# Optimization experiments

Hardware: AMD Instinct MI355X
Metric: run time of the kernel (lower is better)

The kernel has to match this reference:

```python
import jax, jax.numpy as jnp
import numpy as np

B, MENU, N, M = 4096, 256, 8, 16


def setup_inputs() -> dict:
    key = jax.random.key(0)
    k1, k2, k3, k4 = jax.random.split(key, 4)
    input_bids = jax.random.uniform(k1, (B, N, M), dtype=jnp.float32)
    allocs = jax.random.uniform(k2, (B, MENU, N, M), dtype=jnp.float32)
    # bidder weights must be strictly positive (divided by in payments)
    w = jax.random.uniform(k3, (B, N), dtype=jnp.float32, minval=0.5, maxval=1.5)
    b = jax.random.normal(k4, (B, MENU), dtype=jnp.float32)
    softmax_temp = jnp.asarray(100.0, dtype=jnp.float32)
    return {"input_bids": input_bids, "allocs": allocs, "w": w, "b": b,
            "softmax_temp": softmax_temp}


def reference(input_bids, allocs, w, b, softmax_temp):
    Bsz, n, m = input_bids.shape
    # append the "null" menu entry (zero allocation, zero boost)
    allocs = jnp.concatenate([allocs, jnp.zeros((Bsz, 1, n, m), allocs.dtype)], axis=1)  # B,S,n,m
    b = jnp.concatenate([b, jnp.zeros((Bsz, 1), b.dtype)], axis=1)                        # B,S

    # utility of each agent under each menu entry
    util = jnp.einsum('bsnm,bnm->bsn', allocs, input_bids)        # B,S,n
    per_agent_welfare = w[:, None, :] * util                      # B,S,n
    total_welfare = per_agent_welfare.sum(-1)                     # B,S

    alloc_choice = jax.nn.softmax((total_welfare + b) * softmax_temp, axis=-1)  # B,S
    item_allocation = jnp.einsum('bs,bsnm->bnm', alloc_choice, allocs)          # B,n,m
    chosen_welfare = jnp.einsum('bsn,bs->bn', per_agent_welfare, alloc_choice)  # B,n

    # leave-one-out (VCG-style) payments, vectorized over the removed agent i
    mask = 1.0 - jnp.eye(n, dtype=per_agent_welfare.dtype)        # n,n; row i zeros agent i
    removed_welfare = per_agent_welfare[None] * mask[:, None, None, :]  # i,B,S,n
    total_removed = removed_welfare.sum(-1)                       # i,B,S
    removed_choice = jax.nn.softmax((total_removed + b[None]) * softmax_temp, axis=-1)  # i,B,S

    removed_chosen_sum = jnp.einsum('ibsn,ibs->ib', removed_welfare, removed_choice)  # i,B
    masked_chosen_sum = jnp.einsum('bn,in->ib', chosen_welfare, mask)                 # i,B
    removed_b = jnp.einsum('ibs,bs->ib', removed_choice, b)                           # i,B
    alloc_b = jnp.einsum('bs,bs->b', alloc_choice, b)                                 # B

    payments = (removed_chosen_sum + removed_b - masked_chosen_sum - alloc_b[None]) / w.T  # n,B
    return alloc_choice, item_allocation, payments, allocs
```

## Files before the change

### kernel.cpp

```cpp
#include <hip/hip_runtime.h>

#define NAGENTS 8
#define MITEMS 16
#define NM 128
#define MENU 256
#define SFULL 257

__device__ __forceinline__ float wredmax(float v) {
#pragma unroll
    for (int o = 32; o; o >>= 1) v = fmaxf(v, __shfl_xor(v, o));
    return v;
}
__device__ __forceinline__ float wredsum(float v) {
#pragma unroll
    for (int o = 32; o; o >>= 1) v += __shfl_xor(v, o);
    return v;
}

__global__ __launch_bounds__(1024) void cama_kernel(
    const float* __restrict__ bids,
    const float* __restrict__ allocs,
    const float* __restrict__ wvec,
    const float* __restrict__ bvec,
    const float* __restrict__ tempp,
    float* __restrict__ out, int Bsz)
{
    __shared__ float4 lda4[MENU * 32];
    __shared__ float lds_pwT[NAGENTS * MENU];
    __shared__ float lds_tot[MENU];
    __shared__ float lds_bb[MENU];
    __shared__ __align__(16) float lds_bids[NM];
    __shared__ float lds_w[NAGENTS];
    __shared__ float lds_ch[SFULL];
    __shared__ float lds_rcs[NAGENTS], lds_rb[NAGENTS], lds_cw[NAGENTS];
    __shared__ float lds_ab;

    const int u = threadIdx.x;
    const int lane = u & 63;
    const int wave = u >> 6;
    const int b = blockIdx.x;
    const size_t bb = (size_t)b;

    float* out_choice = out;
    float* out_item   = out + (size_t)Bsz * SFULL;
    float* out_pay    = out_item + (size_t)Bsz * NM;
    float* out_all    = out_pay + (size_t)NAGENTS * Bsz;

    if (u < NM) lds_bids[u] = bids[bb * NM + u];
    else if (u < NM + NAGENTS) lds_w[u - NM] = wvec[bb * NAGENTS + (u - NM)];
    if (u >= 256 && u < 512) lds_bb[u - 256] = bvec[bb * MENU + (u - 256)];
    __syncthreads();

    const float temp = tempp[0];
    const int n = u & 7;
    const float w_n = lds_w[n];
    const float4* bq = (const float4*)lds_bids + (n << 2);
    const float4 q0 = bq[0], q1 = bq[1], q2 = bq[2], q3 = bq[3];

#pragma unroll
    for (int i = 0; i < 2; ++i) {
        const int s = (i << 7) + (u >> 3);
        const float4* src = (const float4*)(allocs + ((bb << 8) + s) * NM) + (n << 2);
        float4 a0 = src[0], a1 = src[1], a2 = src[2], a3 = src[3];
        float4* dst = (float4*)(out_all + (bb * SFULL + s) * NM) + (n << 2);
        dst[0] = a0; dst[1] = a1; dst[2] = a2; dst[3] = a3;
        float util = a0.x*q0.x + a0.y*q0.y + a0.z*q0.z + a0.w*q0.w
                   + a1.x*q1.x + a1.y*q1.y + a1.z*q1.z + a1.w*q1.w
                   + a2.x*q2.x + a2.y*q2.y + a2.z*q2.z + a2.w*q2.w
                   + a3.x*q3.x + a3.y*q3.y + a3.z*q3.z + a3.w*q3.w;
        float pwv = w_n * util;
        lds_pwT[(n << 8) + s] = pwv;
        float t4 = pwv;
        t4 += __shfl_xor(t4, 1);
        t4 += __shfl_xor(t4, 2);
        t4 += __shfl_xor(t4, 4);
        if (n == 0) lds_tot[s] = t4;
        const int base = s << 5, c7 = s & 7, j0 = n << 2;
        lda4[base + ((j0 + 0) ^ c7)] = a0;
        lda4[base + ((j0 + 1) ^ c7)] = a1;
        lda4[base + ((j0 + 2) ^ c7)] = a2;
        lda4[base + ((j0 + 3) ^ c7)] = a3;
    }
    if (u < 32) {
        float4 z = make_float4(0.f, 0.f, 0.f, 0.f);
        ((float4*)(out_all + (bb * SFULL + MENU) * NM))[u] = z;
    }
    __syncthreads();

    if (wave == 0) {
        float xs[4], bl[4], es[4];
        float mx = -1e30f;
#pragma unroll
        for (int c = 0; c < 4; ++c) {
            int v = (c << 6) | lane;
            bl[c] = lds_bb[v];
            float x = (lds_tot[v] + bl[c]) * temp;
            xs[c] = x; mx = fmaxf(mx, x);
        }
        mx = fmaxf(wredmax(mx), 0.f);
        float se = 0.f, sab = 0.f;
#pragma unroll
        for (int c = 0; c < 4; ++c) { es[c] = __expf(xs[c] - mx); se += es[c]; sab += es[c] * bl[c]; }
        float en = __expf(-mx);
        se = wredsum(se) + en;
        sab = wredsum(sab);
        float inv = 1.f / se;
#pragma unroll
        for (int c = 0; c < 4; ++c) {
            int v = (c << 6) | lane;
            float chv = es[c] * inv;
            lds_ch[v] = chv;
            out_choice[bb * SFULL + v] = chv;
        }
        if (lane == 0) {
            float chn = en * inv;
            lds_ch[MENU] = chn;
            out_choice[bb * SFULL + MENU] = chn;
            lds_ab = sab * inv;
        }
    } else if (wave <= 8) {
        const int i = wave - 1;
        float xs[4], trs[4], bl[4];
        float mx = -1e30f;
#pragma unroll
        for (int c = 0; c < 4; ++c) {
            int v = (c << 6) | lane;
            bl[c] = lds_bb[v];
            float tr = lds_tot[v] - lds_pwT[(i << 8) + v];
            trs[c] = tr;
            float x = (tr + bl[c]) * temp;
            xs[c] = x; mx = fmaxf(mx, x);
        }
        mx = fmaxf(wredmax(mx), 0.f);
        float se = 0.f, s1 = 0.f, s2 = 0.f;
#pragma unroll
        for (int c = 0; c < 4; ++c) {
            float e = __expf(xs[c] - mx);
            se += e; s1 += e * trs[c]; s2 += e * bl[c];
        }
        se = wredsum(se) + __expf(-mx);
        s1 = wredsum(s1);
        s2 = wredsum(s2);
        if (lane == 0) { lds_rcs[i] = s1 / se; lds_rb[i] = s2 / se; }
    }
    __syncthreads();

    if (wave < 8) {
        float cwv = 0.f;
#pragma unroll
        for (int c = 0; c < 4; ++c) {
            int v = (c << 6) | lane;
            cwv += lds_ch[v] * lds_pwT[(wave << 8) + v];
        }
        cwv = wredsum(cwv);
        if (lane == 0) lds_cw[wave] = cwv;
    }
    {
        const float* ldf = (const float*)lda4;
        const int wl = lane & 7, chunk = lane >> 3;
        const int nm = (wave << 3) + wl;
        const int jj = nm >> 2, r = nm & 3;
        float acc = 0.f;
#pragma unroll 4
        for (int it = 0; it < 32; ++it) {
            int s = (it << 3) + chunk;
            float av = ldf[(((s << 5) + (jj ^ (s & 7))) << 2) + r];
            acc += lds_ch[s] * av;
        }
        acc += __shfl_xor(acc, 8);
        acc += __shfl_xor(acc, 16);
        acc += __shfl_xor(acc, 32);
        if (chunk == 0) out_item[bb * NM + nm] = acc;
    }
    __syncthreads();

    if (u < NAGENTS) {
        float ctot = 0.f;
#pragma unroll
        for (int k = 0; k < NAGENTS; ++k) ctot += lds_cw[k];
        float pay = (lds_rcs[u] + lds_rb[u] - (ctot - lds_cw[u]) - lds_ab) / lds_w[u];
        out_pay[(size_t)u * Bsz + b] = pay;
    }
}

extern "C" void kernel_launch(void* const* d_in, const int* in_sizes, int n_in,
                              void* d_out, int out_size, void* d_ws, size_t ws_size,
                              hipStream_t stream) {
    const float* bids   = (const float*)d_in[0];
    const float* allocs = (const float*)d_in[1];
    const float* wvec   = (const float*)d_in[2];
    const float* bvec   = (const float*)d_in[3];
    const float* tempp  = (const float*)d_in[4];
    float* out = (float*)d_out;
    const int Bsz = in_sizes[0] / (NAGENTS * MITEMS);
    cama_kernel<<<Bsz, 1024, 0, stream>>>(bids, allocs, wvec, bvec, tempp, out, Bsz);
}
```

Before: 268.7 us.

## Halve block size, keep half the menu in registers to shrink LDS

Each block now runs 512 threads instead of 1024. Every thread processes four menu rows instead of two. The first half of the allocation rows stays in registers and is reduced with shuffles into a scratch area, so the shared-memory tile holds only 128 rows and more blocks can fit per CU. The per-agent transposed welfare array gets an XOR swizzle to avoid bank conflicts. All eight waves now run the leave-one-out softmax, the main softmax runs on wave 0 in addition, and the item allocation is finished with an extra cross-wave reduction and barrier. The costs are more register pressure and an extra synchronisation step.

```diff
diff --git a/kernel.cpp b/kernel.cpp
--- a/kernel.cpp
+++ b/kernel.cpp
@@ -17,7 +17,7 @@
     return v;
 }
 
-__global__ __launch_bounds__(1024) void cama_kernel(
+__global__ __launch_bounds__(512, 4) void cama_kernel(
     const float* __restrict__ bids,
     const float* __restrict__ allocs,
     const float* __restrict__ wvec,
@@ -25,7 +25,7 @@
     const float* __restrict__ tempp,
     float* __restrict__ out, int Bsz)
 {
-    __shared__ float4 lda4[MENU * 32];
+    __shared__ float4 lda4[128 * 32];
     __shared__ float lds_pwT[NAGENTS * MENU];
     __shared__ float lds_tot[MENU];
     __shared__ float lds_bb[MENU];
@@ -38,6 +38,8 @@
     const int u = threadIdx.x;
     const int lane = u & 63;
     const int wave = u >> 6;
+    const int n = u & 7;
+    const int sg = u >> 3;
     const int b = blockIdx.x;
     const size_t bb = (size_t)b;
 
@@ -47,19 +49,20 @@
     float* out_all    = out_pay + (size_t)NAGENTS * Bsz;
 
     if (u < NM) lds_bids[u] = bids[bb * NM + u];
-    else if (u < NM + NAGENTS) lds_w[u - NM] = wvec[bb * NAGENTS + (u - NM)];
-    if (u >= 256 && u < 512) lds_bb[u - 256] = bvec[bb * MENU + (u - 256)];
+    if (u >= NM && u < NM + NAGENTS) lds_w[u - NM] = wvec[bb * NAGENTS + (u - NM)];
+    if (u >= 256) lds_bb[u - 256] = bvec[bb * MENU + (u - 256)];
     __syncthreads();
 
     const float temp = tempp[0];
-    const int n = u & 7;
     const float w_n = lds_w[n];
     const float4* bq = (const float4*)lds_bids + (n << 2);
     const float4 q0 = bq[0], q1 = bq[1], q2 = bq[2], q3 = bq[3];
 
-#pragma unroll
-    for (int i = 0; i < 2; ++i) {
-        const int s = (i << 7) + (u >> 3);
+    float4 P00, P01, P02, P03, P10, P11, P12, P13;
+
+#pragma unroll
+    for (int c = 0; c < 4; ++c) {
+        const int s = (c << 6) + sg;
         const float4* src = (const float4*)(allocs + ((bb << 8) + s) * NM) + (n << 2);
         float4 a0 = src[0], a1 = src[1], a2 = src[2], a3 = src[3];
         float4* dst = (float4*)(out_all + (bb * SFULL + s) * NM) + (n << 2);
@@ -69,17 +72,21 @@
                    + a2.x*q2.x + a2.y*q2.y + a2.z*q2.z + a2.w*q2.w
                    + a3.x*q3.x + a3.y*q3.y + a3.z*q3.z + a3.w*q3.w;
         float pwv = w_n * util;
-        lds_pwT[(n << 8) + s] = pwv;
+        lds_pwT[(n << 8) + (s ^ (n << 2))] = pwv;
         float t4 = pwv;
         t4 += __shfl_xor(t4, 1);
         t4 += __shfl_xor(t4, 2);
         t4 += __shfl_xor(t4, 4);
         if (n == 0) lds_tot[s] = t4;
-        const int base = s << 5, c7 = s & 7, j0 = n << 2;
-        lda4[base + ((j0 + 0) ^ c7)] = a0;
-        lda4[base + ((j0 + 1) ^ c7)] = a1;
-        lda4[base + ((j0 + 2) ^ c7)] = a2;
-        lda4[base + ((j0 + 3) ^ c7)] = a3;
+        if (c == 0)      { P00 = a0; P01 = a1; P02 = a2; P03 = a3; }
+        else if (c == 1) { P10 = a0; P11 = a1; P12 = a2; P13 = a3; }
+        else {
+            const int base = (s - 128) << 5, c7 = s & 7, j0 = n << 2;
+            lda4[base + ((j0 + 0) ^ c7)] = a0;
+            lda4[base + ((j0 + 1) ^ c7)] = a1;
+            lda4[base + ((j0 + 2) ^ c7)] = a2;
+            lda4[base + ((j0 + 3) ^ c7)] = a3;
+        }
     }
     if (u < 32) {
         float4 z = make_float4(0.f, 0.f, 0.f, 0.f);
@@ -118,15 +125,16 @@
             out_choice[bb * SFULL + MENU] = chn;
             lds_ab = sab * inv;
         }
-    } else if (wave <= 8) {
-        const int i = wave - 1;
+    }
+    {
+        const int i = wave;
         float xs[4], trs[4], bl[4];
         float mx = -1e30f;
 #pragma unroll
         for (int c = 0; c < 4; ++c) {
             int v = (c << 6) | lane;
             bl[c] = lds_bb[v];
-            float tr = lds_tot[v] - lds_pwT[(i << 8) + v];
+            float tr = lds_tot[v] - lds_pwT[(i << 8) + (v ^ (i << 2))];
             trs[c] = tr;
             float x = (tr + bl[c]) * temp;
             xs[c] = x; mx = fmaxf(mx, x);
@@ -145,35 +153,70 @@
     }
     __syncthreads();
 
-    if (wave < 8) {
+    {
+        const int i = wave;
         float cwv = 0.f;
 #pragma unroll
         for (int c = 0; c < 4; ++c) {
             int v = (c << 6) | lane;
-            cwv += lds_ch[v] * lds_pwT[(wave << 8) + v];
+            cwv += lds_ch[v] * lds_pwT[(i << 8) + (v ^ (i << 2))];
         }
         cwv = wredsum(cwv);
-        if (lane == 0) lds_cw[wave] = cwv;
-    }
-    {
+        if (lane == 0) lds_cw[i] = cwv;
+    }
+    __syncthreads();
+
+    float* scratchA = lds_pwT;
+    float* scratchB = lds_pwT + 1024;
+    {
+        float c0 = lds_ch[sg], c1 = lds_ch[64 + sg];
+        float vs[16];
+        vs[ 0] = P00.x*c0 + P10.x*c1;  vs[ 1] = P00.y*c0 + P10.y*c1;
+        vs[ 2] = P00.z*c0 + P10.z*c1;  vs[ 3] = P00.w*c0 + P10.w*c1;
+        vs[ 4] = P01.x*c0 + P11.x*c1;  vs[ 5] = P01.y*c0 + P11.y*c1;
+        vs[ 6] = P01.z*c0 + P11.z*c1;  vs[ 7] = P01.w*c0 + P11.w*c1;
+        vs[ 8] = P02.x*c0 + P12.x*c1;  vs[ 9] = P02.y*c0 + P12.y*c1;
+        vs[10] = P02.z*c0 + P12.z*c1;  vs[11] = P02.w*c0 + P12.w*c1;
+        vs[12] = P03.x*c0 + P13.x*c1;  vs[13] = P03.y*c0 + P13.y*c1;
+        vs[14] = P03.z*c0 + P13.z*c1;  vs[15] = P03.w*c0 + P13.w*c1;
+#pragma unroll
+        for (int wd = 0; wd < 16; ++wd) {
+            float t = vs[wd];
+            t += __shfl_xor(t, 8);
+            t += __shfl_xor(t, 16);
+            t += __shfl_xor(t, 32);
+            vs[wd] = t;
+        }
+        if (lane < 8) {
+            float4* d4 = (float4*)(scratchA + (wave << 7) + (lane << 4));
+            d4[0] = make_float4(vs[ 0], vs[ 1], vs[ 2], vs[ 3]);
+            d4[1] = make_float4(vs[ 4], vs[ 5], vs[ 6], vs[ 7]);
+            d4[2] = make_float4(vs[ 8], vs[ 9], vs[10], vs[11]);
+            d4[3] = make_float4(vs[12], vs[13], vs[14], vs[15]);
+        }
+    }
+    {
+        const int nm = u & 127, k = u >> 7;
+        const int jj = nm >> 2, r = nm & 3;
         const float* ldf = (const float*)lda4;
-        const int wl = lane & 7, chunk = lane >> 3;
-        const int nm = (wave << 3) + wl;
-        const int jj = nm >> 2, r = nm & 3;
         float acc = 0.f;
-#pragma unroll 4
+#pragma unroll 8
         for (int it = 0; it < 32; ++it) {
-            int s = (it << 3) + chunk;
-            float av = ldf[(((s << 5) + (jj ^ (s & 7))) << 2) + r];
-            acc += lds_ch[s] * av;
-        }
-        acc += __shfl_xor(acc, 8);
-        acc += __shfl_xor(acc, 16);
-        acc += __shfl_xor(acc, 32);
-        if (chunk == 0) out_item[bb * NM + nm] = acc;
-    }
-    __syncthreads();
-
+            int sl = (k << 5) + it;
+            acc += lds_ch[128 + sl] * ldf[(sl << 7) + (((jj ^ (sl & 7)) << 2) | r)];
+        }
+        scratchB[(k << 7) + nm] = acc;
+    }
+    __syncthreads();
+
+    if (u < NM) {
+        float sum = 0.f;
+#pragma unroll
+        for (int w = 0; w < 8; ++w) sum += scratchA[(w << 7) + u];
+#pragma unroll
+        for (int k = 0; k < 4; ++k) sum += scratchB[(k << 7) + u];
+        out_item[bb * NM + u] = sum;
+    }
     if (u < NAGENTS) {
         float ctot = 0.f;
 #pragma unroll
@@ -193,5 +236,5 @@
     const float* tempp  = (const float*)d_in[4];
     float* out = (float*)d_out;
     const int Bsz = in_sizes[0] / (NAGENTS * MITEMS);
-    cama_kernel<<<Bsz, 1024, 0, stream>>>(bids, allocs, wvec, bvec, tempp, out, Bsz);
-}
+    cama_kernel<<<Bsz, 512, 0, stream>>>(bids, allocs, wvec, bvec, tempp, out, Bsz);
+}
```

New measurement: 255.4 us. 4.9% less time.

## Make kernel persistent with register-prefetched next batch and double-buffered LDS

Applied to the files above, without the earlier changes.

Launches a fixed grid of 256 blocks that each loop over consecutive batch elements. While the current element is being processed, the next element's allocs, bids, w and b are loaded into registers, then staged into double-buffered LDS. The goal is to hide global load latency and cut block launch overhead. It also swizzles the lds_pwT index to reduce bank conflicts and replaces __syncthreads with a raw lgkmcnt wait plus s_barrier. In exchange, parallelism drops to 256 blocks on a large GPU, and iters = Bsz/256 silently drops any remainder when B is not a multiple of 256.

```diff
diff --git a/kernel.cpp b/kernel.cpp
--- a/kernel.cpp
+++ b/kernel.cpp
@@ -1,11 +1,12 @@
 #include <hip/hip_runtime.h>
 
 #define NAGENTS 8
-#define MITEMS 16
 #define NM 128
 #define MENU 256
 #define SFULL 257
 
+#define BAR() asm volatile("s_waitcnt lgkmcnt(0)\n\ts_barrier" ::: "memory")
+
 __device__ __forceinline__ float wredmax(float v) {
 #pragma unroll
     for (int o = 32; o; o >>= 1) v = fmaxf(v, __shfl_xor(v, o));
@@ -17,20 +18,20 @@
     return v;
 }
 
-__global__ __launch_bounds__(1024) void cama_kernel(
+__global__ __launch_bounds__(1024, 4) void cama_kernel(
     const float* __restrict__ bids,
     const float* __restrict__ allocs,
     const float* __restrict__ wvec,
     const float* __restrict__ bvec,
     const float* __restrict__ tempp,
-    float* __restrict__ out, int Bsz)
+    float* __restrict__ out, int Bsz, int iters)
 {
     __shared__ float4 lda4[MENU * 32];
     __shared__ float lds_pwT[NAGENTS * MENU];
     __shared__ float lds_tot[MENU];
-    __shared__ float lds_bb[MENU];
-    __shared__ __align__(16) float lds_bids[NM];
-    __shared__ float lds_w[NAGENTS];
+    __shared__ float lds_bb[2][MENU];
+    __shared__ __align__(16) float lds_bids[2][NM];
+    __shared__ float lds_w[2][NAGENTS];
     __shared__ float lds_ch[SFULL];
     __shared__ float lds_rcs[NAGENTS], lds_rb[NAGENTS], lds_cw[NAGENTS];
     __shared__ float lds_ab;
@@ -38,148 +39,208 @@
     const int u = threadIdx.x;
     const int lane = u & 63;
     const int wave = u >> 6;
-    const int b = blockIdx.x;
-    const size_t bb = (size_t)b;
+    const int n = u & 7;
+    const int sg = u >> 3;
 
     float* out_choice = out;
     float* out_item   = out + (size_t)Bsz * SFULL;
     float* out_pay    = out_item + (size_t)Bsz * NM;
     float* out_all    = out_pay + (size_t)NAGENTS * Bsz;
 
-    if (u < NM) lds_bids[u] = bids[bb * NM + u];
-    else if (u < NM + NAGENTS) lds_w[u - NM] = wvec[bb * NAGENTS + (u - NM)];
-    if (u >= 256 && u < 512) lds_bb[u - 256] = bvec[bb * MENU + (u - 256)];
-    __syncthreads();
-
     const float temp = tempp[0];
-    const int n = u & 7;
-    const float w_n = lds_w[n];
-    const float4* bq = (const float4*)lds_bids + (n << 2);
-    const float4 q0 = bq[0], q1 = bq[1], q2 = bq[2], q3 = bq[3];
-
-#pragma unroll
-    for (int i = 0; i < 2; ++i) {
-        const int s = (i << 7) + (u >> 3);
-        const float4* src = (const float4*)(allocs + ((bb << 8) + s) * NM) + (n << 2);
-        float4 a0 = src[0], a1 = src[1], a2 = src[2], a3 = src[3];
-        float4* dst = (float4*)(out_all + (bb * SFULL + s) * NM) + (n << 2);
-        dst[0] = a0; dst[1] = a1; dst[2] = a2; dst[3] = a3;
-        float util = a0.x*q0.x + a0.y*q0.y + a0.z*q0.z + a0.w*q0.w
-                   + a1.x*q1.x + a1.y*q1.y + a1.z*q1.z + a1.w*q1.w
-                   + a2.x*q2.x + a2.y*q2.y + a2.z*q2.z + a2.w*q2.w
-                   + a3.x*q3.x + a3.y*q3.y + a3.z*q3.z + a3.w*q3.w;
-        float pwv = w_n * util;
-        lds_pwT[(n << 8) + s] = pwv;
-        float t4 = pwv;
-        t4 += __shfl_xor(t4, 1);
-        t4 += __shfl_xor(t4, 2);
-        t4 += __shfl_xor(t4, 4);
-        if (n == 0) lds_tot[s] = t4;
-        const int base = s << 5, c7 = s & 7, j0 = n << 2;
-        lda4[base + ((j0 + 0) ^ c7)] = a0;
-        lda4[base + ((j0 + 1) ^ c7)] = a1;
-        lda4[base + ((j0 + 2) ^ c7)] = a2;
-        lda4[base + ((j0 + 3) ^ c7)] = a3;
+
+    size_t a = (size_t)blockIdx.x * iters;
+
+    float Pf[2][16];
+
+    {
+        float rbb = 0.f, rbid = 0.f, rw = 0.f;
+        if (u < MENU)    rbb  = bvec[a * MENU + u];
+        if (u < NM)      rbid = bids[a * NM + u];
+        if (u < NAGENTS) rw   = wvec[a * NAGENTS + u];
+        const float4* s0 = (const float4*)(allocs + (a * MENU + sg) * NM) + (n << 2);
+        const float4* s1 = (const float4*)(allocs + (a * MENU + 128 + sg) * NM) + (n << 2);
+        float4 a0 = s0[0], a1 = s0[1], a2 = s0[2], a3 = s0[3];
+        float4 b0 = s1[0], b1 = s1[1], b2 = s1[2], b3 = s1[3];
+        Pf[0][0]=a0.x;  Pf[0][1]=a0.y;  Pf[0][2]=a0.z;  Pf[0][3]=a0.w;
+        Pf[0][4]=a1.x;  Pf[0][5]=a1.y;  Pf[0][6]=a1.z;  Pf[0][7]=a1.w;
+        Pf[0][8]=a2.x;  Pf[0][9]=a2.y;  Pf[0][10]=a2.z; Pf[0][11]=a2.w;
+        Pf[0][12]=a3.x; Pf[0][13]=a3.y; Pf[0][14]=a3.z; Pf[0][15]=a3.w;
+        Pf[1][0]=b0.x;  Pf[1][1]=b0.y;  Pf[1][2]=b0.z;  Pf[1][3]=b0.w;
+        Pf[1][4]=b1.x;  Pf[1][5]=b1.y;  Pf[1][6]=b1.z;  Pf[1][7]=b1.w;
+        Pf[1][8]=b2.x;  Pf[1][9]=b2.y;  Pf[1][10]=b2.z; Pf[1][11]=b2.w;
+        Pf[1][12]=b3.x; Pf[1][13]=b3.y; Pf[1][14]=b3.z; Pf[1][15]=b3.w;
+        if (u < MENU)    lds_bb[0][u]   = rbb;
+        if (u < NM)      lds_bids[0][u] = rbid;
+        if (u < NAGENTS) lds_w[0][u]    = rw;
     }
-    if (u < 32) {
-        float4 z = make_float4(0.f, 0.f, 0.f, 0.f);
-        ((float4*)(out_all + (bb * SFULL + MENU) * NM))[u] = z;
-    }
-    __syncthreads();
-
-    if (wave == 0) {
-        float xs[4], bl[4], es[4];
-        float mx = -1e30f;
-#pragma unroll
-        for (int c = 0; c < 4; ++c) {
-            int v = (c << 6) | lane;
-            bl[c] = lds_bb[v];
-            float x = (lds_tot[v] + bl[c]) * temp;
-            xs[c] = x; mx = fmaxf(mx, x);
-        }
-        mx = fmaxf(wredmax(mx), 0.f);
-        float se = 0.f, sab = 0.f;
-#pragma unroll
-        for (int c = 0; c < 4; ++c) { es[c] = __expf(xs[c] - mx); se += es[c]; sab += es[c] * bl[c]; }
-        float en = __expf(-mx);
-        se = wredsum(se) + en;
-        sab = wredsum(sab);
-        float inv = 1.f / se;
-#pragma unroll
-        for (int c = 0; c < 4; ++c) {
-            int v = (c << 6) | lane;
-            float chv = es[c] * inv;
-            lds_ch[v] = chv;
-            out_choice[bb * SFULL + v] = chv;
-        }
-        if (lane == 0) {
-            float chn = en * inv;
-            lds_ch[MENU] = chn;
-            out_choice[bb * SFULL + MENU] = chn;
-            lds_ab = sab * inv;
-        }
-    } else if (wave <= 8) {
-        const int i = wave - 1;
-        float xs[4], trs[4], bl[4];
-        float mx = -1e30f;
-#pragma unroll
-        for (int c = 0; c < 4; ++c) {
-            int v = (c << 6) | lane;
-            bl[c] = lds_bb[v];
-            float tr = lds_tot[v] - lds_pwT[(i << 8) + v];
-            trs[c] = tr;
-            float x = (tr + bl[c]) * temp;
-            xs[c] = x; mx = fmaxf(mx, x);
-        }
-        mx = fmaxf(wredmax(mx), 0.f);
-        float se = 0.f, s1 = 0.f, s2 = 0.f;
-#pragma unroll
-        for (int c = 0; c < 4; ++c) {
-            float e = __expf(xs[c] - mx);
-            se += e; s1 += e * trs[c]; s2 += e * bl[c];
-        }
-        se = wredsum(se) + __expf(-mx);
-        s1 = wredsum(s1);
-        s2 = wredsum(s2);
-        if (lane == 0) { lds_rcs[i] = s1 / se; lds_rb[i] = s2 / se; }
-    }
-    __syncthreads();
-
-    if (wave < 8) {
-        float cwv = 0.f;
-#pragma unroll
-        for (int c = 0; c < 4; ++c) {
-            int v = (c << 6) | lane;
-            cwv += lds_ch[v] * lds_pwT[(wave << 8) + v];
-        }
-        cwv = wredsum(cwv);
-        if (lane == 0) lds_cw[wave] = cwv;
-    }
-    {
-        const float* ldf = (const float*)lda4;
-        const int wl = lane & 7, chunk = lane >> 3;
-        const int nm = (wave << 3) + wl;
-        const int jj = nm >> 2, r = nm & 3;
-        float acc = 0.f;
-#pragma unroll 4
-        for (int it = 0; it < 32; ++it) {
-            int s = (it << 3) + chunk;
-            float av = ldf[(((s << 5) + (jj ^ (s & 7))) << 2) + r];
-            acc += lds_ch[s] * av;
-        }
-        acc += __shfl_xor(acc, 8);
-        acc += __shfl_xor(acc, 16);
-        acc += __shfl_xor(acc, 32);
-        if (chunk == 0) out_item[bb * NM + nm] = acc;
-    }
-    __syncthreads();
-
-    if (u < NAGENTS) {
-        float ctot = 0.f;
-#pragma unroll
-        for (int k = 0; k < NAGENTS; ++k) ctot += lds_cw[k];
-        float pay = (lds_rcs[u] + lds_rb[u] - (ctot - lds_cw[u]) - lds_ab) / lds_w[u];
-        out_pay[(size_t)u * Bsz + b] = pay;
+    BAR();
+
+    for (int it = 0; it < iters; ++it) {
+        const int p = it & 1;
+
+        float qf[16];
+        {
+            const float4* bq = (const float4*)(&lds_bids[p][0]) + (n << 2);
+            float4 qa = bq[0], qb = bq[1], qc = bq[2], qd = bq[3];
+            qf[0]=qa.x; qf[1]=qa.y; qf[2]=qa.z; qf[3]=qa.w;
+            qf[4]=qb.x; qf[5]=qb.y; qf[6]=qb.z; qf[7]=qb.w;
+            qf[8]=qc.x; qf[9]=qc.y; qf[10]=qc.z; qf[11]=qc.w;
+            qf[12]=qd.x; qf[13]=qd.y; qf[14]=qd.z; qf[15]=qd.w;
+        }
+        const float w_n = lds_w[p][n];
+#pragma unroll
+        for (int c = 0; c < 2; ++c) {
+            const int s = (c << 7) + sg;
+            float4 v0 = make_float4(Pf[c][0],  Pf[c][1],  Pf[c][2],  Pf[c][3]);
+            float4 v1 = make_float4(Pf[c][4],  Pf[c][5],  Pf[c][6],  Pf[c][7]);
+            float4 v2 = make_float4(Pf[c][8],  Pf[c][9],  Pf[c][10], Pf[c][11]);
+            float4 v3 = make_float4(Pf[c][12], Pf[c][13], Pf[c][14], Pf[c][15]);
+            float4* dst = (float4*)(out_all + (a * SFULL + s) * NM) + (n << 2);
+            dst[0] = v0; dst[1] = v1; dst[2] = v2; dst[3] = v3;
+            float util = 0.f;
+#pragma unroll
+            for (int k = 0; k < 16; ++k) util += Pf[c][k] * qf[k];
+            float pwv = w_n * util;
+            lds_pwT[(n << 8) + (s ^ (n << 2))] = pwv;
+            float t4 = pwv;
+            t4 += __shfl_xor(t4, 1);
+            t4 += __shfl_xor(t4, 2);
+            t4 += __shfl_xor(t4, 4);
+            if (n == 0) lds_tot[s] = t4;
+            const int base = s << 5, c7 = s & 7, j0 = n << 2;
+            lda4[base + ((j0 + 0) ^ c7)] = v0;
+            lda4[base + ((j0 + 1) ^ c7)] = v1;
+            lda4[base + ((j0 + 2) ^ c7)] = v2;
+            lda4[base + ((j0 + 3) ^ c7)] = v3;
+        }
+        if (u < 32)
+            ((float4*)(out_all + (a * SFULL + MENU) * NM))[u] =
+                make_float4(0.f, 0.f, 0.f, 0.f);
+
+        const bool has_next = (it + 1 < iters);
+        const size_t an = a + 1;
+        float rbb2 = 0.f, rbid2 = 0.f, rw2 = 0.f;
+        if (has_next) {
+            if (u < MENU)    rbb2  = bvec[an * MENU + u];
+            if (u < NM)      rbid2 = bids[an * NM + u];
+            if (u < NAGENTS) rw2   = wvec[an * NAGENTS + u];
+            const float4* s0 = (const float4*)(allocs + (an * MENU + sg) * NM) + (n << 2);
+            const float4* s1 = (const float4*)(allocs + (an * MENU + 128 + sg) * NM) + (n << 2);
+            float4 a0 = s0[0], a1 = s0[1], a2 = s0[2], a3 = s0[3];
+            float4 b0 = s1[0], b1 = s1[1], b2 = s1[2], b3 = s1[3];
+            Pf[0][0]=a0.x;  Pf[0][1]=a0.y;  Pf[0][2]=a0.z;  Pf[0][3]=a0.w;
+            Pf[0][4]=a1.x;  Pf[0][5]=a1.y;  Pf[0][6]=a1.z;  Pf[0][7]=a1.w;
+            Pf[0][8]=a2.x;  Pf[0][9]=a2.y;  Pf[0][10]=a2.z; Pf[0][11]=a2.w;
+            Pf[0][12]=a3.x; Pf[0][13]=a3.y; Pf[0][14]=a3.z; Pf[0][15]=a3.w;
+            Pf[1][0]=b0.x;  Pf[1][1]=b0.y;  Pf[1][2]=b0.z;  Pf[1][3]=b0.w;
+            Pf[1][4]=b1.x;  Pf[1][5]=b1.y;  Pf[1][6]=b1.z;  Pf[1][7]=b1.w;
+            Pf[1][8]=b2.x;  Pf[1][9]=b2.y;  Pf[1][10]=b2.z; Pf[1][11]=b2.w;
+            Pf[1][12]=b3.x; Pf[1][13]=b3.y; Pf[1][14]=b3.z; Pf[1][15]=b3.w;
+        }
+        BAR();
+
+        if (wave == 0) {
+            float xs[4], bl[4], es[4];
+            float mx = -1e30f;
+#pragma unroll
+            for (int c = 0; c < 4; ++c) {
+                int v = (c << 6) | lane;
+                bl[c] = lds_bb[p][v];
+                float x = (lds_tot[v] + bl[c]) * temp;
+                xs[c] = x; mx = fmaxf(mx, x);
+            }
+            mx = fmaxf(wredmax(mx), 0.f);
+            float se = 0.f, sab = 0.f;
+#pragma unroll
+            for (int c = 0; c < 4; ++c) { es[c] = __expf(xs[c] - mx); se += es[c]; sab += es[c] * bl[c]; }
+            float en = __expf(-mx);
+            se = wredsum(se) + en;
+            sab = wredsum(sab);
+            float inv = 1.f / se;
+#pragma unroll
+            for (int c = 0; c < 4; ++c) {
+                int v = (c << 6) | lane;
+                float chv = es[c] * inv;
+                lds_ch[v] = chv;
+                out_choice[a * SFULL + v] = chv;
+            }
+            if (lane == 0) {
+                float chn = en * inv;
+                lds_ch[MENU] = chn;
+                out_choice[a * SFULL + MENU] = chn;
+                lds_ab = sab * inv;
+            }
+        } else if (wave <= 8) {
+            const int i = wave - 1;
+            float xs[4], trs[4], bl[4];
+            float mx = -1e30f;
+#pragma unroll
+            for (int c = 0; c < 4; ++c) {
+                int v = (c << 6) | lane;
+                bl[c] = lds_bb[p][v];
+                float tr = lds_tot[v] - lds_pwT[(i << 8) + (v ^ (i << 2))];
+                trs[c] = tr;
+                float x = (tr + bl[c]) * temp;
+                xs[c] = x; mx = fmaxf(mx, x);
+            }
+            mx = fmaxf(wredmax(mx), 0.f);
+            float se = 0.f, s1 = 0.f, s2 = 0.f;
+#pragma unroll
+            for (int c = 0; c < 4; ++c) {
+                float e = __expf(xs[c] - mx);
+                se += e; s1 += e * trs[c]; s2 += e * bl[c];
+            }
+            se = wredsum(se) + __expf(-mx);
+            s1 = wredsum(s1);
+            s2 = wredsum(s2);
+            if (lane == 0) { lds_rcs[i] = s1 / se; lds_rb[i] = s2 / se; }
+        }
+        BAR();
+
+        if (wave < 8) {
+            const int i = wave;
+            float cwv = 0.f;
+#pragma unroll
+            for (int c = 0; c < 4; ++c) {
+                int v = (c << 6) | lane;
+                cwv += lds_ch[v] * lds_pwT[(i << 8) + (v ^ (i << 2))];
+            }
+            cwv = wredsum(cwv);
+            if (lane == 0) lds_cw[i] = cwv;
+        }
+        {
+            const float* ldf = (const float*)lda4;
+            const int wl = lane & 7, chunk = lane >> 3;
+            const int nm = (wave << 3) + wl;
+            const int jj = nm >> 2, r = nm & 3;
+            float acc = 0.f;
+#pragma unroll 8
+            for (int it2 = 0; it2 < 32; ++it2) {
+                int s = (it2 << 3) + chunk;
+                acc += lds_ch[s] * ldf[(((s << 5) + (jj ^ (s & 7))) << 2) + r];
+            }
+            acc += __shfl_xor(acc, 8);
+            acc += __shfl_xor(acc, 16);
+            acc += __shfl_xor(acc, 32);
+            if (chunk == 0) out_item[a * NM + nm] = acc;
+        }
+        if (has_next) {
+            if (u < MENU)    lds_bb[p ^ 1][u]   = rbb2;
+            if (u < NM)      lds_bids[p ^ 1][u] = rbid2;
+            if (u < NAGENTS) lds_w[p ^ 1][u]    = rw2;
+        }
+        BAR();
+
+        if (u < NAGENTS) {
+            float ctot = 0.f;
+#pragma unroll
+            for (int k = 0; k < NAGENTS; ++k) ctot += lds_cw[k];
+            float pay = (lds_rcs[u] + lds_rb[u] - (ctot - lds_cw[u]) - lds_ab)
+                        / lds_w[p][u];
+            out_pay[(size_t)u * Bsz + a] = pay;
+        }
+        a = an;
     }
 }
 
@@ -192,6 +253,9 @@
     const float* bvec   = (const float*)d_in[3];
     const float* tempp  = (const float*)d_in[4];
     float* out = (float*)d_out;
-    const int Bsz = in_sizes[0] / (NAGENTS * MITEMS);
-    cama_kernel<<<Bsz, 1024, 0, stream>>>(bids, allocs, wvec, bvec, tempp, out, Bsz);
-}
+    const int Bsz = in_sizes[0] / NM;
+    const int nblocks = 256;
+    const int iters = Bsz / nblocks;
+    cama_kernel<<<nblocks, 1024, 0, stream>>>(bids, allocs, wvec, bvec, tempp,
+                                              out, Bsz, iters);
+}
```

Result: no change. 267.9 us (-0.3%).
